# Performance work log

Hardware: AMD Instinct MI355X
Metric: run time of the kernel (lower is better)

Reference implementation:

```python
import jax, jax.numpy as jnp
import numpy as np

INF = jnp.float32(np.inf)
LAMBDA_VAL = 1.0
NUM_CLASSES = 10

def setup_inputs() -> dict:
    key = jax.random.key(0)
    k1, k2, k3 = jax.random.split(key, 3)
    N, P, D = 65536, 2048, 64
    x = jax.random.normal(k1, (N, D), dtype=jnp.float32)
    y = jax.random.randint(k2, (N,), 0, NUM_CLASSES)
    prototypes = jax.random.normal(k3, (P, D), dtype=jnp.float32)
    prototype_labels = jnp.arange(P) % NUM_CLASSES
    return {"x": x, "y": y, "prototypes": prototypes, "prototype_labels": prototype_labels}

def _cdist(x, p):
    # Euclidean pairwise distances via the gemm expansion (matches torch.cdist default
    x2 = jnp.sum(x * x, axis=1, keepdims=True)          # [N, 1]
    p2 = jnp.sum(p * p, axis=1)                          # [P]
    sq = x2 + p2[None, :] - 2.0 * (x @ p.T)              # [N, P]
    return jnp.sqrt(jnp.maximum(sq, 0.0))

def reference(x, y, prototypes, prototype_labels):
    distances = _cdist(x, prototypes)                    # [N, P]
    same = prototype_labels[None, :] == y[:, None]       # [N, P] bool
    pos = jnp.min(jnp.where(same, distances, INF), axis=1)   # [N]
    neg = jnp.min(jnp.where(~same, distances, INF), axis=1)  # [N]
    mu = (pos - neg) / (pos + neg)
    loss = jnp.mean(jax.nn.sigmoid(LAMBDA_VAL * mu))
    return loss
```

## Files before the change

kernel.cpp:

```cpp
#include <hip/hip_runtime.h>
#include <math.h>

#define NROWS  65536
#define NPROTO 2048
#define DDIM   64
#define NCLS   10

#define NPROTO_PAD 2560
#define CHUNK_BYTES 8448

#define WS_IMG_BYTES   (40 * CHUNK_BYTES)
#define WS_MINS_OFF    WS_IMG_BYTES
#define WS_MINS_BYTES  (NCLS * NROWS * 2)
#define WS_X2_OFF      (WS_MINS_OFF + WS_MINS_BYTES)

typedef __attribute__((ext_vector_type(8))) short bf16x8;
typedef __attribute__((ext_vector_type(4))) float f32x4;
typedef __attribute__((ext_vector_type(4))) unsigned int u32x4;

__device__ inline unsigned int f2bf(float f) {
    unsigned int u = __float_as_uint(f);
    return (u + 0x7FFFu + ((u >> 16) & 1u)) >> 16;
}

template <int CTRL>
__device__ inline float rorMin(float v) {
    int t = __builtin_amdgcn_update_dpp(0, __float_as_int(v), CTRL, 0xF, 0xF, false);
    return fminf(v, __int_as_float(t));
}

__global__ __launch_bounds__(256) void convert_kernel(
        const float* __restrict__ protos, char* __restrict__ wsB,
        float* __restrict__ out) {
    int t = blockIdx.x * 256 + threadIdx.x;
    int s = t >> 3, jj = t & 7;
    int L = s >> 8, j = s & 255;
    int cnt = (L < 8) ? 205 : 204;
    bool real = (j < cnt);
    float v[8] = {0.f, 0.f, 0.f, 0.f, 0.f, 0.f, 0.f, 0.f};
    if (real) {
        const float* src = protos + (L + 10 * j) * DDIM + jj * 8;
        float4 a = *(const float4*)src;
        float4 b = *(const float4*)(src + 4);
        v[0] = a.x; v[1] = a.y; v[2] = a.z; v[3] = a.w;
        v[4] = b.x; v[5] = b.y; v[6] = b.z; v[7] = b.w;
    }
    float ss = 0.f;
#pragma unroll
    for (int i = 0; i < 8; i++) ss = fmaf(v[i], v[i], ss);
    ss += __shfl_xor(ss, 1, 64);
    ss += __shfl_xor(ss, 2, 64);
    ss += __shfl_xor(ss, 4, 64);
    unsigned int w[4];
#pragma unroll
    for (int i = 0; i < 4; i++) {
        unsigned int lo = f2bf(-2.f * v[2 * i]);
        unsigned int hi = f2bf(-2.f * v[2 * i + 1]);
        w[i] = lo | (hi << 16);
    }
    int c = s >> 6, r = s & 63;
    size_t off = (size_t)c * CHUNK_BYTES + (size_t)(r * 8 + (jj ^ (r & 7))) * 16;
    *(u32x4*)(wsB + off) = (u32x4){w[0], w[1], w[2], w[3]};
    if (jj == 0)
        *(float*)(wsB + (size_t)c * CHUNK_BYTES + 8192 + r * 4) =
            real ? ss : __builtin_inff();
    if (t == 0) out[0] = 0.f;
}

__global__ __launch_bounds__(256) void x2_kernel(const float* __restrict__ x,
                                                 float* __restrict__ wsX2) {
    int t = blockIdx.x * 256 + threadIdx.x;
    int row = t >> 4, j = t & 15;
    float4 v = ((const float4*)(x + (size_t)row * DDIM))[j];
    float s = v.x * v.x;
    s = fmaf(v.y, v.y, s);
    s = fmaf(v.z, v.z, s);
    s = fmaf(v.w, v.w, s);
    s += __shfl_xor(s, 1, 64);
    s += __shfl_xor(s, 2, 64);
    s += __shfl_xor(s, 4, 64);
    s += __shfl_xor(s, 8, 64);
    if (j == 0) wsX2[row] = s;
}

__global__ __launch_bounds__(512, 4) void glvq_main(
        const float* __restrict__ x, const char* __restrict__ wsB,
        _Float16* __restrict__ wsMins) {
    __shared__ __align__(16) char ldsImg[8][CHUNK_BYTES];

    const int tid  = threadIdx.x;
    const int wave = tid >> 6;
    const int lane = tid & 63;
    const int quad = lane >> 4;
    const int l15  = lane & 15;
    const int piece = blockIdx.y;
    const float CINF = __builtin_inff();

    {
        const char* src = wsB + (size_t)(piece * 8 + wave) * CHUNK_BYTES;
        char* dst = ldsImg[wave];
#pragma unroll
        for (int i = 0; i < 8; i++)
            __builtin_amdgcn_global_load_lds(
                (const __attribute__((address_space(1))) void*)(src + i * 1024 + lane * 16),
                (__attribute__((address_space(3))) void*)(dst + i * 1024),
                16, 0, 0);
        __builtin_amdgcn_global_load_lds(
            (const __attribute__((address_space(1))) void*)(src + 8192 + lane * 4),
            (__attribute__((address_space(3))) void*)(dst + 8192),
            4, 0, 0);
    }
    asm volatile("s_waitcnt vmcnt(0)" ::: "memory");
    __syncthreads();

    const int rowBase = (blockIdx.x * 8 + wave) * 64;
    bf16x8 afrag[4][2];
#pragma unroll
    for (int m = 0; m < 4; m++) {
        const float* xr = x + (size_t)(rowBase + m * 16 + l15) * DDIM;
#pragma unroll
        for (int k = 0; k < 2; k++) {
            const float* sp = xr + k * 32 + quad * 8;
            float4 u0 = *(const float4*)sp;
            float4 u1 = *(const float4*)(sp + 4);
            float vv[8] = {u0.x, u0.y, u0.z, u0.w, u1.x, u1.y, u1.z, u1.w};
            bf16x8 af;
#pragma unroll
            for (int i = 0; i < 8; i++) af[i] = (short)f2bf(vv[i]);
            afrag[m][k] = af;
        }
    }

#pragma unroll
    for (int ph = 0; ph < 2; ph++) {
        float mMin[4][4];
#pragma unroll
        for (int m = 0; m < 4; m++)
#pragma unroll
            for (int r = 0; r < 4; r++) mMin[m][r] = CINF;

#pragma unroll
        for (int c = 0; c < 4; c++) {
            const char* buf = ldsImg[ph * 4 + c];
#pragma unroll
            for (int fg = 0; fg < 2; fg++) {
                const int fA = fg * 2, fB = fg * 2 + 1;
                float p2a = *(const float*)(buf + 8192 + (fA * 16 + l15) * 4);
                float p2b = *(const float*)(buf + 8192 + (fB * 16 + l15) * 4);
                f32x4 acc[4][2];
#pragma unroll
                for (int m = 0; m < 4; m++) {
                    acc[m][0] = (f32x4){p2a, p2a, p2a, p2a};
                    acc[m][1] = (f32x4){p2b, p2b, p2b, p2b};
                }
#pragma unroll
                for (int k = 0; k < 2; k++) {
                    bf16x8 bA = *(const bf16x8*)(buf +
                        ((fA * 16 + l15) * 8 + ((k * 4 + quad) ^ (l15 & 7))) * 16);
                    bf16x8 bB = *(const bf16x8*)(buf +
                        ((fB * 16 + l15) * 8 + ((k * 4 + quad) ^ (l15 & 7))) * 16);
#pragma unroll
                    for (int m = 0; m < 4; m++) {
                        acc[m][0] = __builtin_amdgcn_mfma_f32_16x16x32_bf16(
                            afrag[m][k], bA, acc[m][0], 0, 0, 0);
                        acc[m][1] = __builtin_amdgcn_mfma_f32_16x16x32_bf16(
                            afrag[m][k], bB, acc[m][1], 0, 0, 0);
                    }
                }
#pragma unroll
                for (int m = 0; m < 4; m++)
#pragma unroll
                    for (int r = 0; r < 4; r++)
                        mMin[m][r] = fminf(fminf(acc[m][0][r], acc[m][1][r]),
                                           mMin[m][r]);
            }
        }

#pragma unroll
        for (int m = 0; m < 4; m++)
#pragma unroll
            for (int r = 0; r < 4; r++) {
                float v = mMin[m][r];
                v = rorMin<0x128>(v);
                v = rorMin<0x124>(v);
                v = rorMin<0x122>(v);
                v = rorMin<0x121>(v);
                mMin[m][r] = v;
            }

        if (l15 == 0) {
            _Float16* plane = wsMins + (size_t)(piece * 2 + ph) * NROWS + rowBase;
#pragma unroll
            for (int m = 0; m < 4; m++)
#pragma unroll
                for (int r = 0; r < 4; r++)
                    plane[m * 16 + quad * 4 + r] = (_Float16)mMin[m][r];
        }
    }
}

__global__ __launch_bounds__(256) void combine_kernel(
        const int* __restrict__ y, const _Float16* __restrict__ wsMins,
        const float* __restrict__ wsX2, float* __restrict__ out) {
    int row = blockIdx.x * 256 + threadIdx.x;
    int yr = y[row];
    float pos = 0.f, neg = __builtin_inff();
#pragma unroll
    for (int L = 0; L < NCLS; L++) {
        float d = (float)wsMins[(size_t)L * NROWS + row];
        bool isPos = (L == yr);
        pos = isPos ? d : pos;
        neg = isPos ? neg : fminf(neg, d);
    }
    float x2v = wsX2[row];
    float sp = sqrtf(fmaxf(x2v + pos, 0.f));
    float sn = sqrtf(fmaxf(x2v + neg, 0.f));
    float mu = (sp - sn) / (sp + sn);
    float s = 1.f / (1.f + __expf(-mu));

    __shared__ float red[256];
    red[threadIdx.x] = s;
    __syncthreads();
#pragma unroll
    for (int off = 128; off > 0; off >>= 1) {
        if (threadIdx.x < off) red[threadIdx.x] += red[threadIdx.x + off];
        __syncthreads();
    }
    if (threadIdx.x == 0) atomicAdd(out, red[0] * (1.f / (float)NROWS));
}

extern "C" void kernel_launch(void* const* d_in, const int* in_sizes, int n_in,
                              void* d_out, int out_size, void* d_ws, size_t ws_size,
                              hipStream_t stream) {
    const float* x      = (const float*)d_in[0];
    const int*   y      = (const int*)d_in[1];
    const float* protos = (const float*)d_in[2];
    float* out = (float*)d_out;

    char*      wsB    = (char*)d_ws;
    _Float16*  wsMins = (_Float16*)((char*)d_ws + WS_MINS_OFF);
    float*     wsX2   = (float*)((char*)d_ws + WS_X2_OFF);

    convert_kernel<<<NPROTO_PAD * 8 / 256, 256, 0, stream>>>(protos, wsB, out);
    x2_kernel<<<NROWS * 16 / 256, 256, 0, stream>>>(x, wsX2);
    glvq_main<<<dim3(128, 5), 512, 0, stream>>>(x, wsB, wsMins);
    combine_kernel<<<NROWS / 256, 256, 0, stream>>>(y, wsMins, wsX2, out);
}
```

Before: 108.6 us.

## Pre-convert x to bf16 MFMA fragment layout in merged prep kernel

Merges the prototype conversion and x-norm kernels into one prep kernel that also converts x to bf16 and writes it in the exact per-lane MFMA A-fragment layout. The main kernel then loads its fragments with one coalesced 16-byte load each, issued before the LDS prototype load, instead of reading fp32 rows five times (once per grid column) and converting them. This removes one launch and redundant fp32 reads and conversions, at the cost of an extra 8 MB workspace write and read pass.

```diff
diff --git a/kernel.cpp b/kernel.cpp
--- a/kernel.cpp
+++ b/kernel.cpp
@@ -10,7 +10,9 @@
 #define CHUNK_BYTES 8448
 
 #define WS_IMG_BYTES   (40 * CHUNK_BYTES)
-#define WS_MINS_OFF    WS_IMG_BYTES
+#define WS_XA_OFF      WS_IMG_BYTES
+#define WS_XA_BYTES    (1024 * 8192)
+#define WS_MINS_OFF    (WS_XA_OFF + WS_XA_BYTES)
 #define WS_MINS_BYTES  (NCLS * NROWS * 2)
 #define WS_X2_OFF      (WS_MINS_OFF + WS_MINS_BYTES)
 
@@ -29,63 +31,73 @@
     return fminf(v, __int_as_float(t));
 }
 
-__global__ __launch_bounds__(256) void convert_kernel(
-        const float* __restrict__ protos, char* __restrict__ wsB,
-        float* __restrict__ out) {
-    int t = blockIdx.x * 256 + threadIdx.x;
-    int s = t >> 3, jj = t & 7;
-    int L = s >> 8, j = s & 255;
-    int cnt = (L < 8) ? 205 : 204;
-    bool real = (j < cnt);
-    float v[8] = {0.f, 0.f, 0.f, 0.f, 0.f, 0.f, 0.f, 0.f};
-    if (real) {
-        const float* src = protos + (L + 10 * j) * DDIM + jj * 8;
+__global__ __launch_bounds__(256) void prep_kernel(
+        const float* __restrict__ x, const float* __restrict__ protos,
+        char* __restrict__ wsB, float* __restrict__ out) {
+    if (blockIdx.x < 80) {
+        int t = blockIdx.x * 256 + threadIdx.x;
+        int s = t >> 3, jj = t & 7;
+        int L = s >> 8, j = s & 255;
+        int cnt = (L < 8) ? 205 : 204;
+        bool real = (j < cnt);
+        float v[8] = {0.f, 0.f, 0.f, 0.f, 0.f, 0.f, 0.f, 0.f};
+        if (real) {
+            const float* src = protos + (L + 10 * j) * DDIM + jj * 8;
+            float4 a = *(const float4*)src;
+            float4 b = *(const float4*)(src + 4);
+            v[0] = a.x; v[1] = a.y; v[2] = a.z; v[3] = a.w;
+            v[4] = b.x; v[5] = b.y; v[6] = b.z; v[7] = b.w;
+        }
+        float ss = 0.f;
+#pragma unroll
+        for (int i = 0; i < 8; i++) ss = fmaf(v[i], v[i], ss);
+        ss += __shfl_xor(ss, 1, 64);
+        ss += __shfl_xor(ss, 2, 64);
+        ss += __shfl_xor(ss, 4, 64);
+        unsigned int w[4];
+#pragma unroll
+        for (int i = 0; i < 4; i++) {
+            unsigned int lo = f2bf(-2.f * v[2 * i]);
+            unsigned int hi = f2bf(-2.f * v[2 * i + 1]);
+            w[i] = lo | (hi << 16);
+        }
+        int c = s >> 6, r = s & 63;
+        size_t off = (size_t)c * CHUNK_BYTES + (size_t)(r * 8 + (jj ^ (r & 7))) * 16;
+        *(u32x4*)(wsB + off) = (u32x4){w[0], w[1], w[2], w[3]};
+        if (jj == 0)
+            *(float*)(wsB + (size_t)c * CHUNK_BYTES + 8192 + r * 4) =
+                real ? ss : __builtin_inff();
+        if (t == 0) out[0] = 0.f;
+    } else {
+        int t = (blockIdx.x - 80) * 256 + threadIdx.x;
+        int row = t >> 3, j = t & 7;
+        const float* src = x + (size_t)row * DDIM + j * 8;
         float4 a = *(const float4*)src;
         float4 b = *(const float4*)(src + 4);
-        v[0] = a.x; v[1] = a.y; v[2] = a.z; v[3] = a.w;
-        v[4] = b.x; v[5] = b.y; v[6] = b.z; v[7] = b.w;
-    }
-    float ss = 0.f;
-#pragma unroll
-    for (int i = 0; i < 8; i++) ss = fmaf(v[i], v[i], ss);
-    ss += __shfl_xor(ss, 1, 64);
-    ss += __shfl_xor(ss, 2, 64);
-    ss += __shfl_xor(ss, 4, 64);
-    unsigned int w[4];
-#pragma unroll
-    for (int i = 0; i < 4; i++) {
-        unsigned int lo = f2bf(-2.f * v[2 * i]);
-        unsigned int hi = f2bf(-2.f * v[2 * i + 1]);
-        w[i] = lo | (hi << 16);
-    }
-    int c = s >> 6, r = s & 63;
-    size_t off = (size_t)c * CHUNK_BYTES + (size_t)(r * 8 + (jj ^ (r & 7))) * 16;
-    *(u32x4*)(wsB + off) = (u32x4){w[0], w[1], w[2], w[3]};
-    if (jj == 0)
-        *(float*)(wsB + (size_t)c * CHUNK_BYTES + 8192 + r * 4) =
-            real ? ss : __builtin_inff();
-    if (t == 0) out[0] = 0.f;
-}
-
-__global__ __launch_bounds__(256) void x2_kernel(const float* __restrict__ x,
-                                                 float* __restrict__ wsX2) {
-    int t = blockIdx.x * 256 + threadIdx.x;
-    int row = t >> 4, j = t & 15;
-    float4 v = ((const float4*)(x + (size_t)row * DDIM))[j];
-    float s = v.x * v.x;
-    s = fmaf(v.y, v.y, s);
-    s = fmaf(v.z, v.z, s);
-    s = fmaf(v.w, v.w, s);
-    s += __shfl_xor(s, 1, 64);
-    s += __shfl_xor(s, 2, 64);
-    s += __shfl_xor(s, 4, 64);
-    s += __shfl_xor(s, 8, 64);
-    if (j == 0) wsX2[row] = s;
+        float v[8] = {a.x, a.y, a.z, a.w, b.x, b.y, b.z, b.w};
+        float ss = 0.f;
+#pragma unroll
+        for (int i = 0; i < 8; i++) ss = fmaf(v[i], v[i], ss);
+        ss += __shfl_xor(ss, 1, 64);
+        ss += __shfl_xor(ss, 2, 64);
+        ss += __shfl_xor(ss, 4, 64);
+        unsigned int w[4];
+#pragma unroll
+        for (int i = 0; i < 4; i++) {
+            unsigned int lo = f2bf(v[2 * i]);
+            unsigned int hi = f2bf(v[2 * i + 1]);
+            w[i] = lo | (hi << 16);
+        }
+        int rt = row >> 6, m = (row & 63) >> 4, l15 = row & 15;
+        int k = j >> 2, q = j & 3;
+        size_t off = (size_t)rt * 8192 + m * 2048 + k * 1024 + (q * 16 + l15) * 16;
+        *(u32x4*)(wsB + WS_XA_OFF + off) = (u32x4){w[0], w[1], w[2], w[3]};
+        if (j == 0) *(float*)(wsB + WS_X2_OFF + (size_t)row * 4) = ss;
+    }
 }
 
 __global__ __launch_bounds__(512, 4) void glvq_main(
-        const float* __restrict__ x, const char* __restrict__ wsB,
-        _Float16* __restrict__ wsMins) {
+        const char* __restrict__ wsB, _Float16* __restrict__ wsMins) {
     __shared__ __align__(16) char ldsImg[8][CHUNK_BYTES];
 
     const int tid  = threadIdx.x;
@@ -95,6 +107,15 @@
     const int l15  = lane & 15;
     const int piece = blockIdx.y;
     const float CINF = __builtin_inff();
+
+    const int rowTile = blockIdx.x * 8 + wave;
+    const char* xATile = wsB + WS_XA_OFF + (size_t)rowTile * 8192;
+    bf16x8 afrag[4][2];
+#pragma unroll
+    for (int m = 0; m < 4; m++)
+#pragma unroll
+        for (int k = 0; k < 2; k++)
+            afrag[m][k] = *(const bf16x8*)(xATile + m * 2048 + k * 1024 + lane * 16);
 
     {
         const char* src = wsB + (size_t)(piece * 8 + wave) * CHUNK_BYTES;
@@ -113,23 +134,7 @@
     asm volatile("s_waitcnt vmcnt(0)" ::: "memory");
     __syncthreads();
 
-    const int rowBase = (blockIdx.x * 8 + wave) * 64;
-    bf16x8 afrag[4][2];
-#pragma unroll
-    for (int m = 0; m < 4; m++) {
-        const float* xr = x + (size_t)(rowBase + m * 16 + l15) * DDIM;
-#pragma unroll
-        for (int k = 0; k < 2; k++) {
-            const float* sp = xr + k * 32 + quad * 8;
-            float4 u0 = *(const float4*)sp;
-            float4 u1 = *(const float4*)(sp + 4);
-            float vv[8] = {u0.x, u0.y, u0.z, u0.w, u1.x, u1.y, u1.z, u1.w};
-            bf16x8 af;
-#pragma unroll
-            for (int i = 0; i < 8; i++) af[i] = (short)f2bf(vv[i]);
-            afrag[m][k] = af;
-        }
-    }
+    const int rowBase = rowTile * 64;
 
 #pragma unroll
     for (int ph = 0; ph < 2; ph++) {
@@ -241,8 +246,7 @@
     _Float16*  wsMins = (_Float16*)((char*)d_ws + WS_MINS_OFF);
     float*     wsX2   = (float*)((char*)d_ws + WS_X2_OFF);
 
-    convert_kernel<<<NPROTO_PAD * 8 / 256, 256, 0, stream>>>(protos, wsB, out);
-    x2_kernel<<<NROWS * 16 / 256, 256, 0, stream>>>(x, wsX2);
-    glvq_main<<<dim3(128, 5), 512, 0, stream>>>(x, wsB, wsMins);
+    prep_kernel<<<80 + NROWS * 8 / 256, 256, 0, stream>>>(x, protos, wsB, out);
+    glvq_main<<<dim3(128, 5), 512, 0, stream>>>(wsB, wsMins);
     combine_kernel<<<NROWS / 256, 256, 0, stream>>>(y, wsMins, wsX2, out);
 }
```

Result: faster. 98.72 us (-9.1%).
